# Optimization experiments

Hardware: AMD Instinct MI355X
Metric: run time of the kernel (lower is better)

Reference implementation:

```python
import jax, jax.numpy as jnp
import numpy as np

B, D_IN, H, D_OUT, E = 16384, 512, 1024, 512, 4


def setup_inputs() -> dict:
    key = jax.random.key(0)
    ks = jax.random.split(key, 8)
    x = jax.random.normal(ks[0], (B, D_IN), dtype=jnp.float32)
    command = jax.random.randint(ks[1], (B,), 0, E, dtype=jnp.int64)
    # Per-branch Encoder params: Linear(D_IN->H), Linear(H->H), Linear(H->D_OUT)
    s = 0.02
    W1 = jax.random.normal(ks[2], (E, D_IN, H), dtype=jnp.float32) * s
    b1 = jnp.zeros((E, H), dtype=jnp.float32)
    W2 = jax.random.normal(ks[3], (E, H, H), dtype=jnp.float32) * s
    b2 = jnp.zeros((E, H), dtype=jnp.float32)
    W3 = jax.random.normal(ks[4], (E, H, D_OUT), dtype=jnp.float32) * s
    b3 = jnp.zeros((E, D_OUT), dtype=jnp.float32)
    return {"x": x, "command": command, "W1": W1, "b1": b1,
            "W2": W2, "b2": b2, "W3": W3, "b3": b3}


def reference(x, command, W1, b1, W2, b2, W3, b3):
    # Evaluate all branches as batched GEMMs, then select per-sample branch.
    # Mathematically identical to per-sample dispatch in the torch module.
    h = jax.nn.relu(jnp.einsum('bi,eih->beh', x, W1) + b1)        # [B,E,H]
    h = jax.nn.relu(jnp.einsum('beh,ehk->bek', h, W2) + b2)       # [B,E,H]
    y = jnp.tanh(jnp.einsum('bek,eko->beo', h, W3) + b3)          # [B,E,D_OUT]
    # select branch output per sample according to command
    idx = command.astype(jnp.int32)[:, None, None]                # [B,1,1]
    out = jnp.take_along_axis(y, idx, axis=1)[:, 0, :]            # [B,D_OUT]
    return out
```

## Files before the change

### kernel.cpp

```cpp
#include <hip/hip_runtime.h>


#define B_N   16384
#define DIN   512
#define HID   1024
#define DOUT  512
#define MAXTILES 136

typedef __attribute__((ext_vector_type(8))) short bf16x8;
typedef __attribute__((ext_vector_type(4))) float f32x4;
typedef __attribute__((address_space(3))) unsigned int lds_u32;
typedef const __attribute__((address_space(1))) unsigned int glb_u32;

__device__ __forceinline__ void gll16(const void* g, void* l) {
    __builtin_amdgcn_global_load_lds((glb_u32*)g, (lds_u32*)l, 16, 0, 0);
}

__device__ __forceinline__ unsigned short f2bf(float f) {
    unsigned int u = __float_as_uint(f);
    u += 0x7FFFu + ((u >> 16) & 1u);
    return (unsigned short)(u >> 16);
}

__device__ __forceinline__ float fast_tanh(float x) {
    x = fminf(fmaxf(x, -9.0f), 9.0f);
    float t = __builtin_amdgcn_exp2f(x * 2.8853900817779268f);
    return (t - 1.0f) * __builtin_amdgcn_rcpf(t + 1.0f);
}

__global__ void plan_all_k(const int* __restrict__ cmd, int* __restrict__ ctrl,
                           int* __restrict__ tileExpert, int* __restrict__ tileBase) {
    __shared__ int h[4];
    int tid = threadIdx.x;
    if (tid < 4) h[tid] = 0;
    __syncthreads();
    int c0 = 0, c1 = 0, c2 = 0, c3 = 0;
    for (int i = tid; i < B_N; i += 256) {
        int e = cmd[i] & 3;
        c0 += (e == 0); c1 += (e == 1); c2 += (e == 2); c3 += (e == 3);
    }
    atomicAdd(&h[0], c0); atomicAdd(&h[1], c1);
    atomicAdd(&h[2], c2); atomicAdd(&h[3], c3);
    __syncthreads();
    if (tid == 0) {
        int P = 0, nt = 0;
        for (int e = 0; e < 4; ++e) {
            ctrl[e] = h[e];
            ctrl[4 + e] = 0;
            ctrl[8 + e] = P;
            int tiles = (h[e] + 127) >> 7;
            for (int t = 0; t < tiles; ++t) {
                tileExpert[nt] = e;
                tileBase[nt] = P + t * 128;
                ++nt;
            }
            P += tiles * 128;
        }
        ctrl[12] = P;
        ctrl[13] = nt;
    }
}

__global__ void scatter_k(const int* __restrict__ cmd, int* __restrict__ ctrl,
                          int* __restrict__ perm) {
    int i = blockIdx.x * 256 + threadIdx.x;
    int e = cmd[i] & 3;
    int lane = threadIdx.x & 63;
#pragma unroll
    for (int ee = 0; ee < 4; ++ee) {
        unsigned long long mask = __ballot(e == ee);
        if (e == ee) {
            int leader = __ffsll((unsigned long long)mask) - 1;
            int rank = __popcll(mask & ((1ull << lane) - 1ull));
            int wbase = 0;
            if (lane == leader)
                wbase = atomicAdd(&ctrl[4 + ee], __popcll(mask));
            wbase = __builtin_amdgcn_readfirstlane(wbase);
            perm[ctrl[8 + ee] + wbase + rank] = i;
        }
    }
}

__global__ __launch_bounds__(256) void prep_data_k(
    const float* __restrict__ W1, const float* __restrict__ W2,
    const float* __restrict__ W3, unsigned short* __restrict__ Wt1,
    unsigned short* __restrict__ Wt2, unsigned short* __restrict__ Wt3,
    const float* __restrict__ x, unsigned short* __restrict__ xp,
    int* __restrict__ perm, const int* __restrict__ ctrl)
{
    int b = blockIdx.x;
    if (b < 8192) {
        int e = b >> 11, r = b & 2047;
        const float* W; unsigned short* Wt; int KD, ND, kt, nt;
        if (r < 512)       { W = W1; Wt = Wt1; KD = 512;  ND = 1024; kt = r & 15;           nt = r >> 4; }
        else if (r < 1536) { W = W2; Wt = Wt2; KD = 1024; ND = 1024; kt = (r - 512) & 31;   nt = (r - 512) >> 5; }
        else               { W = W3; Wt = Wt3; KD = 1024; ND = 512;  kt = (r - 1536) & 31;  nt = (r - 1536) >> 5; }
        __shared__ float t[32][33];
        size_t base = (size_t)e * KD * ND;
        int k0 = kt * 32, n0 = nt * 32;
        int tx = threadIdx.x & 31, ty = threadIdx.x >> 5;
#pragma unroll
        for (int s = 0; s < 4; ++s)
            t[ty + s * 8][tx] = W[base + (size_t)(k0 + ty + s * 8) * ND + n0 + tx];
        __syncthreads();
#pragma unroll
        for (int s = 0; s < 4; ++s)
            Wt[base + (size_t)(n0 + ty + s * 8) * KD + k0 + tx] = f2bf(t[tx][ty + s * 8]);
    } else {
        int g = b - 8192;
        int p = g * 4 + (int)(threadIdx.x >> 6);
        if (p >= ctrl[12]) return;
        int lane = threadIdx.x & 63;
        int e = (p >= ctrl[9]) + (p >= ctrl[10]) + (p >= ctrl[11]);
        int segBase = ctrl[8 + e];
        int src;
        if (p < segBase + ctrl[e]) {
            src = perm[p];
        } else {
            src = perm[segBase];
            if (lane == 0) perm[p] = src;
        }
        const float* xr = x + (size_t)src * DIN + lane * 8;
        float4 a = *(const float4*)xr;
        float4 c = *(const float4*)(xr + 4);
        uint4 o;
        o.x = (unsigned)f2bf(a.x) | ((unsigned)f2bf(a.y) << 16);
        o.y = (unsigned)f2bf(a.z) | ((unsigned)f2bf(a.w) << 16);
        o.z = (unsigned)f2bf(c.x) | ((unsigned)f2bf(c.y) << 16);
        o.w = (unsigned)f2bf(c.z) | ((unsigned)f2bf(c.w) << 16);
        *(uint4*)(xp + (size_t)p * DIN + lane * 8) = o;
    }
}

template<int K, int N, int ACT, bool SCATTER_OUT>
__global__ __launch_bounds__(512) void gemm_k(
    const unsigned short* __restrict__ A, const unsigned short* __restrict__ Bt,
    const float* __restrict__ bias, void* __restrict__ Outp,
    const int* __restrict__ ctrl, const int* __restrict__ tileExpert,
    const int* __restrict__ tileBase, const int* __restrict__ perm)
{
    if ((int)blockIdx.x >= ctrl[13]) return;
    const int e = tileExpert[blockIdx.x];
    const int rowBase = tileBase[blockIdx.x];
    const int n0 = blockIdx.y * 256;

    __shared__ unsigned short Als[128 * 32];
    __shared__ unsigned short Bls[256 * 32];

    const int tid = threadIdx.x;
    const int lane = tid & 63;
    const int w = tid >> 6;
    const int wm = w >> 2, wn = w & 3;
    const int lr = lane & 15, lh = lane >> 4;

    f32x4 acc[4][4] = {};

    const int sr = tid >> 2;
    const int sc = (tid & 3) * 8;
    const unsigned short* Ab = A + (size_t)rowBase * K;
    const unsigned short* Bb = Bt + ((size_t)e * N + n0) * K;

    for (int kb = 0; kb < K / 32; ++kb) {
        const int k0 = kb * 32;
        __syncthreads();
        gll16(Ab + (size_t)sr * K + k0 + sc, &Als[sr * 32 + sc]);
        gll16(Bb + (size_t)sr * K + k0 + sc, &Bls[sr * 32 + sc]);
        gll16(Bb + (size_t)(sr + 128) * K + k0 + sc, &Bls[(sr + 128) * 32 + sc]);
        __syncthreads();
        bf16x8 afr[4], bfr[4];
#pragma unroll
        for (int mi = 0; mi < 4; ++mi)
            afr[mi] = *(const bf16x8*)&Als[(wm * 64 + mi * 16 + lr) * 32 + lh * 8];
#pragma unroll
        for (int ni = 0; ni < 4; ++ni)
            bfr[ni] = *(const bf16x8*)&Bls[(wn * 64 + ni * 16 + lr) * 32 + lh * 8];
#pragma unroll
        for (int mi = 0; mi < 4; ++mi)
#pragma unroll
            for (int ni = 0; ni < 4; ++ni)
                acc[mi][ni] = __builtin_amdgcn_mfma_f32_16x16x32_bf16(
                    afr[mi], bfr[ni], acc[mi][ni], 0, 0, 0);
    }

    float bv[4];
    int colv[4];
#pragma unroll
    for (int ni = 0; ni < 4; ++ni) {
        colv[ni] = n0 + wn * 64 + ni * 16 + lr;
        bv[ni] = bias[e * N + colv[ni]];
    }
#pragma unroll
    for (int mi = 0; mi < 4; ++mi) {
#pragma unroll
        for (int r = 0; r < 4; ++r) {
            int rowL = wm * 64 + mi * 16 + lh * 4 + r;
            int gRow = rowBase + rowL;
            int orow = SCATTER_OUT ? perm[gRow] : gRow;
#pragma unroll
            for (int ni = 0; ni < 4; ++ni) {
                float v = acc[mi][ni][r] + bv[ni];
                if (ACT == 0) v = fmaxf(v, 0.0f);
                else          v = fast_tanh(v);
                if (SCATTER_OUT)
                    ((float*)Outp)[(size_t)orow * N + colv[ni]] = v;
                else
                    ((unsigned short*)Outp)[(size_t)orow * N + colv[ni]] = f2bf(v);
            }
        }
    }
}

extern "C" void kernel_launch(void* const* d_in, const int* in_sizes, int n_in,
                              void* d_out, int out_size, void* d_ws, size_t ws_size,
                              hipStream_t stream) {
    const float* x  = (const float*)d_in[0];
    const int*   cmd= (const int*)d_in[1];
    const float* W1 = (const float*)d_in[2];
    const float* b1 = (const float*)d_in[3];
    const float* W2 = (const float*)d_in[4];
    const float* b2 = (const float*)d_in[5];
    const float* W3 = (const float*)d_in[6];
    const float* b3 = (const float*)d_in[7];
    float* out = (float*)d_out;

    char* w = (char*)d_ws;
    int* ctrl       = (int*)w;
    int* tileExpert = ctrl + 64;
    int* tileBase   = ctrl + 224;
    int* perm       = ctrl + 512;
    unsigned short* Wt1 = (unsigned short*)(w + 131072);
    unsigned short* Wt2 = (unsigned short*)(w + 131072 + 4194304);
    unsigned short* Wt3 = (unsigned short*)(w + 131072 + 12582912);
    unsigned short* h1  = (unsigned short*)(w + 131072 + 16777216);
    unsigned short* h2  = h1 + (size_t)16896 * HID;
    unsigned short* xp  = h2;

    plan_all_k<<<1, 256, 0, stream>>>(cmd, ctrl, tileExpert, tileBase);
    scatter_k<<<B_N / 256, 256, 0, stream>>>(cmd, ctrl, perm);
    prep_data_k<<<8192 + 4224, 256, 0, stream>>>(W1, W2, W3, Wt1, Wt2, Wt3,
                                                 x, xp, perm, ctrl);

    gemm_k<DIN, HID, 0, false><<<dim3(MAXTILES, 4), 512, 0, stream>>>(
        xp, Wt1, b1, h1, ctrl, tileExpert, tileBase, perm);
    gemm_k<HID, HID, 0, false><<<dim3(MAXTILES, 4), 512, 0, stream>>>(
        h1, Wt2, b2, h2, ctrl, tileExpert, tileBase, perm);
    gemm_k<HID, DOUT, 1, true><<<dim3(MAXTILES, 2), 512, 0, stream>>>(
        h2, Wt3, b3, out, ctrl, tileExpert, tileBase, perm);
}
```

Before: 195.1 us.

## Double-buffer LDS tiles and shrink GEMM blocks to 128x128 with 256 threads

The grouped GEMM kernel now prefetches the next K-slice into a second LDS buffer while computing on the current one. This replaces the two barriers per iteration with a single waitcnt plus barrier. Block tiles shrink from 128x256 with 512 threads to 128x128 with 256 threads, and the grid's N dimension doubles. The goal is to hide global-load latency and raise the number of resident blocks per CU. The cost is more blocks re-reading the A tiles, and the waitcnt(0) still stalls on the prefetch at the start of each iteration.

```diff
diff --git a/kernel.cpp b/kernel.cpp
--- a/kernel.cpp
+++ b/kernel.cpp
@@ -133,7 +133,7 @@
 }
 
 template<int K, int N, int ACT, bool SCATTER_OUT>
-__global__ __launch_bounds__(512) void gemm_k(
+__global__ __launch_bounds__(256) void gemm_k(
     const unsigned short* __restrict__ A, const unsigned short* __restrict__ Bt,
     const float* __restrict__ bias, void* __restrict__ Outp,
     const int* __restrict__ ctrl, const int* __restrict__ tileExpert,
@@ -142,38 +142,52 @@
     if ((int)blockIdx.x >= ctrl[13]) return;
     const int e = tileExpert[blockIdx.x];
     const int rowBase = tileBase[blockIdx.x];
-    const int n0 = blockIdx.y * 256;
-
-    __shared__ unsigned short Als[128 * 32];
-    __shared__ unsigned short Bls[256 * 32];
+    const int n0 = blockIdx.y * 128;
+
+    __shared__ unsigned short Als[2][128 * 32];
+    __shared__ unsigned short Bls[2][128 * 32];
 
     const int tid = threadIdx.x;
     const int lane = tid & 63;
     const int w = tid >> 6;
-    const int wm = w >> 2, wn = w & 3;
+    const int wm = w >> 1, wn = w & 1;
     const int lr = lane & 15, lh = lane >> 4;
 
     f32x4 acc[4][4] = {};
 
     const int sr = tid >> 2;
     const int sc = (tid & 3) * 8;
-    const unsigned short* Ab = A + (size_t)rowBase * K;
-    const unsigned short* Bb = Bt + ((size_t)e * N + n0) * K;
-
-    for (int kb = 0; kb < K / 32; ++kb) {
-        const int k0 = kb * 32;
-        __syncthreads();
-        gll16(Ab + (size_t)sr * K + k0 + sc, &Als[sr * 32 + sc]);
-        gll16(Bb + (size_t)sr * K + k0 + sc, &Bls[sr * 32 + sc]);
-        gll16(Bb + (size_t)(sr + 128) * K + k0 + sc, &Bls[(sr + 128) * 32 + sc]);
-        __syncthreads();
+    const int l1 = sr * 32 + sc;
+    const int l2 = (sr + 64) * 32 + sc;
+    const unsigned short* Ab1 = A + (size_t)(rowBase + sr) * K + sc;
+    const unsigned short* Ab2 = A + (size_t)(rowBase + sr + 64) * K + sc;
+    const unsigned short* Bb1 = Bt + ((size_t)e * N + n0 + sr) * K + sc;
+    const unsigned short* Bb2 = Bt + ((size_t)e * N + n0 + sr + 64) * K + sc;
+
+    constexpr int NK = K / 32;
+#define STAGE(buf, kb) do {                                   \
+        const int _k0 = (kb) * 32;                            \
+        gll16(Ab1 + _k0, &Als[buf][l1]);                      \
+        gll16(Ab2 + _k0, &Als[buf][l2]);                      \
+        gll16(Bb1 + _k0, &Bls[buf][l1]);                      \
+        gll16(Bb2 + _k0, &Bls[buf][l2]);                      \
+    } while (0)
+
+    STAGE(0, 0);
+#pragma unroll 2
+    for (int kb = 0; kb < NK; ++kb) {
+        const int cur = kb & 1;
+        asm volatile("s_waitcnt vmcnt(0)" ::: "memory");
+        __builtin_amdgcn_s_barrier();
+        asm volatile("" ::: "memory");
+        if (kb + 1 < NK) STAGE(cur ^ 1, kb + 1);
         bf16x8 afr[4], bfr[4];
 #pragma unroll
         for (int mi = 0; mi < 4; ++mi)
-            afr[mi] = *(const bf16x8*)&Als[(wm * 64 + mi * 16 + lr) * 32 + lh * 8];
+            afr[mi] = *(const bf16x8*)&Als[cur][(wm * 64 + mi * 16 + lr) * 32 + lh * 8];
 #pragma unroll
         for (int ni = 0; ni < 4; ++ni)
-            bfr[ni] = *(const bf16x8*)&Bls[(wn * 64 + ni * 16 + lr) * 32 + lh * 8];
+            bfr[ni] = *(const bf16x8*)&Bls[cur][(wn * 64 + ni * 16 + lr) * 32 + lh * 8];
 #pragma unroll
         for (int mi = 0; mi < 4; ++mi)
 #pragma unroll
@@ -181,6 +195,7 @@
                 acc[mi][ni] = __builtin_amdgcn_mfma_f32_16x16x32_bf16(
                     afr[mi], bfr[ni], acc[mi][ni], 0, 0, 0);
     }
+#undef STAGE
 
     float bv[4];
     int colv[4];
@@ -240,10 +255,10 @@
     prep_data_k<<<8192 + 4224, 256, 0, stream>>>(W1, W2, W3, Wt1, Wt2, Wt3,
                                                  x, xp, perm, ctrl);
 
-    gemm_k<DIN, HID, 0, false><<<dim3(MAXTILES, 4), 512, 0, stream>>>(
+    gemm_k<DIN, HID, 0, false><<<dim3(MAXTILES, 8), 256, 0, stream>>>(
         xp, Wt1, b1, h1, ctrl, tileExpert, tileBase, perm);
-    gemm_k<HID, HID, 0, false><<<dim3(MAXTILES, 4), 512, 0, stream>>>(
+    gemm_k<HID, HID, 0, false><<<dim3(MAXTILES, 8), 256, 0, stream>>>(
         h1, Wt2, b2, h2, ctrl, tileExpert, tileBase, perm);
-    gemm_k<HID, DOUT, 1, true><<<dim3(MAXTILES, 2), 512, 0, stream>>>(
+    gemm_k<HID, DOUT, 1, true><<<dim3(MAXTILES, 4), 256, 0, stream>>>(
         h2, Wt3, b3, out, ctrl, tileExpert, tileBase, perm);
 }
```

Result: faster. 186.3 us (-4.5%).

## Retile grouped GEMM to 128x128 blocks with K=64 stages and XOR-swizzled LDS

Applied to the files above, without the earlier changes.

Each GEMM block now computes a 128x128 tile with 4 waves (256 threads) instead of 128x256 with 8 waves, and each stage loads a K-slice of 64 instead of 32, halving the number of barrier pairs per tile. LDS rows are XOR-swizzled on 16-byte chunks to avoid bank conflicts on the fragment reads. Grid width along N doubles to keep coverage. The smaller tile means less reuse of the A tile per block and more blocks reading the same A rows, and it remains single-buffered with no overlap of loads and MFMA.

```diff
diff --git a/kernel.cpp b/kernel.cpp
--- a/kernel.cpp
+++ b/kernel.cpp
@@ -133,7 +133,7 @@
 }
 
 template<int K, int N, int ACT, bool SCATTER_OUT>
-__global__ __launch_bounds__(512) void gemm_k(
+__global__ __launch_bounds__(256) void gemm_k(
     const unsigned short* __restrict__ A, const unsigned short* __restrict__ Bt,
     const float* __restrict__ bias, void* __restrict__ Outp,
     const int* __restrict__ ctrl, const int* __restrict__ tileExpert,
@@ -142,44 +142,53 @@
     if ((int)blockIdx.x >= ctrl[13]) return;
     const int e = tileExpert[blockIdx.x];
     const int rowBase = tileBase[blockIdx.x];
-    const int n0 = blockIdx.y * 256;
-
-    __shared__ unsigned short Als[128 * 32];
-    __shared__ unsigned short Bls[256 * 32];
+    const int n0 = blockIdx.y * 128;
+
+    __shared__ unsigned short Als[128 * 64];
+    __shared__ unsigned short Bls[128 * 64];
 
     const int tid = threadIdx.x;
     const int lane = tid & 63;
     const int w = tid >> 6;
-    const int wm = w >> 2, wn = w & 3;
+    const int wm = w >> 1, wn = w & 1;
     const int lr = lane & 15, lh = lane >> 4;
 
     f32x4 acc[4][4] = {};
 
-    const int sr = tid >> 2;
-    const int sc = (tid & 3) * 8;
-    const unsigned short* Ab = A + (size_t)rowBase * K;
-    const unsigned short* Bb = Bt + ((size_t)e * N + n0) * K;
-
-    for (int kb = 0; kb < K / 32; ++kb) {
-        const int k0 = kb * 32;
+    const int tr = tid >> 3;
+    const int tc = tid & 7;
+    const int cs = (tc ^ (tr & 7)) * 8;
+    const unsigned short* As = A + (size_t)(rowBase + tr) * K + cs;
+    const unsigned short* Bs = Bt + ((size_t)e * N + n0 + tr) * K + cs;
+    const int ldst = tr * 64 + tc * 8;
+
+    constexpr int NK = K / 64;
+    for (int kq = 0; kq < NK; ++kq) {
+        const int k0 = kq * 64;
         __syncthreads();
-        gll16(Ab + (size_t)sr * K + k0 + sc, &Als[sr * 32 + sc]);
-        gll16(Bb + (size_t)sr * K + k0 + sc, &Bls[sr * 32 + sc]);
-        gll16(Bb + (size_t)(sr + 128) * K + k0 + sc, &Bls[(sr + 128) * 32 + sc]);
+#pragma unroll
+        for (int j = 0; j < 4; ++j) {
+            gll16(As + (size_t)(j * 32) * K + k0, &Als[j * 2048 + ldst]);
+            gll16(Bs + (size_t)(j * 32) * K + k0, &Bls[j * 2048 + ldst]);
+        }
         __syncthreads();
-        bf16x8 afr[4], bfr[4];
-#pragma unroll
-        for (int mi = 0; mi < 4; ++mi)
-            afr[mi] = *(const bf16x8*)&Als[(wm * 64 + mi * 16 + lr) * 32 + lh * 8];
-#pragma unroll
-        for (int ni = 0; ni < 4; ++ni)
-            bfr[ni] = *(const bf16x8*)&Bls[(wn * 64 + ni * 16 + lr) * 32 + lh * 8];
-#pragma unroll
-        for (int mi = 0; mi < 4; ++mi)
+#pragma unroll
+        for (int kk = 0; kk < 2; ++kk) {
+            const int ksl = ((kk * 4 + lh) ^ (lr & 7)) * 8;
+            bf16x8 afr[4], bfr[4];
+#pragma unroll
+            for (int mi = 0; mi < 4; ++mi)
+                afr[mi] = *(const bf16x8*)&Als[(wm * 64 + mi * 16 + lr) * 64 + ksl];
 #pragma unroll
             for (int ni = 0; ni < 4; ++ni)
-                acc[mi][ni] = __builtin_amdgcn_mfma_f32_16x16x32_bf16(
-                    afr[mi], bfr[ni], acc[mi][ni], 0, 0, 0);
+                bfr[ni] = *(const bf16x8*)&Bls[(wn * 64 + ni * 16 + lr) * 64 + ksl];
+#pragma unroll
+            for (int mi = 0; mi < 4; ++mi)
+#pragma unroll
+                for (int ni = 0; ni < 4; ++ni)
+                    acc[mi][ni] = __builtin_amdgcn_mfma_f32_16x16x32_bf16(
+                        afr[mi], bfr[ni], acc[mi][ni], 0, 0, 0);
+        }
     }
 
     float bv[4];
@@ -240,10 +249,10 @@
     prep_data_k<<<8192 + 4224, 256, 0, stream>>>(W1, W2, W3, Wt1, Wt2, Wt3,
                                                  x, xp, perm, ctrl);
 
-    gemm_k<DIN, HID, 0, false><<<dim3(MAXTILES, 4), 512, 0, stream>>>(
+    gemm_k<DIN, HID, 0, false><<<dim3(MAXTILES, 8), 256, 0, stream>>>(
         xp, Wt1, b1, h1, ctrl, tileExpert, tileBase, perm);
-    gemm_k<HID, HID, 0, false><<<dim3(MAXTILES, 4), 512, 0, stream>>>(
+    gemm_k<HID, HID, 0, false><<<dim3(MAXTILES, 8), 256, 0, stream>>>(
         h1, Wt2, b2, h2, ctrl, tileExpert, tileBase, perm);
-    gemm_k<HID, DOUT, 1, true><<<dim3(MAXTILES, 2), 512, 0, stream>>>(
+    gemm_k<HID, DOUT, 1, true><<<dim3(MAXTILES, 4), 256, 0, stream>>>(
         h2, Wt3, b3, out, ctrl, tileExpert, tileBase, perm);
 }
```

After: 167.9 us. -13.9%, faster.
